# Performance work log

Hardware: AMD Instinct MI355X
Metric: run time of the kernel (lower is better)

Reference implementation:

```python
import jax, jax.numpy as jnp
import numpy as np

DIM = 1024
HEADS = 16
HEAD_DIM = DIM // HEADS          # 64
ROT_DIM = max(16, HEAD_DIM // 2) # 32 (already even)
B, S = 1, 2048


def _linear_params(key, scale=0.02):
    w = jax.random.normal(key, (DIM, DIM), dtype=jnp.float32) * scale
    b = jnp.zeros((DIM,), dtype=jnp.float32)
    return w, b


def setup_inputs() -> dict:
    key = jax.random.key(0)
    ks = jax.random.split(key, 16)
    real = jax.random.normal(ks[0], (B, S, DIM), dtype=jnp.float32)
    imag = jax.random.normal(ks[1], (B, S, DIM), dtype=jnp.float32)
    Wq_r, bq_r = _linear_params(ks[2])
    Wk_r, bk_r = _linear_params(ks[3])
    Wv_r, bv_r = _linear_params(ks[4])
    Wq_i, bq_i = _linear_params(ks[5])
    Wk_i, bk_i = _linear_params(ks[6])
    Wv_i, bv_i = _linear_params(ks[7])
    Wo_r, bo_r = _linear_params(ks[8])
    Wo_i, bo_i = _linear_params(ks[9])
    phase_shifts = jax.random.normal(ks[10], (HEADS, HEAD_DIM), dtype=jnp.float32) * 0.02
    # entanglement init: 0.8*I + 0.1 on super/sub diagonal + 0.1 corners
    ent = np.eye(HEADS, dtype=np.float32) * 0.8
    ent += np.diag(np.ones(HEADS - 1, dtype=np.float32) * 0.1, k=1)
    ent += np.diag(np.ones(HEADS - 1, dtype=np.float32) * 0.1, k=-1)
    ent[0, -1] = 0.1
    ent[-1, 0] = 0.1
    entanglement_matrix = jnp.asarray(ent)
    exponent = np.arange(0, ROT_DIM, 2, dtype=np.float64) / ROT_DIM
    rotary_freqs = jnp.asarray((10000.0 ** (-exponent)).astype(np.float32))
    return {
        'real': real, 'imag': imag,
        'Wq_r': Wq_r, 'bq_r': bq_r, 'Wk_r': Wk_r, 'bk_r': bk_r,
        'Wv_r': Wv_r, 'bv_r': bv_r, 'Wq_i': Wq_i, 'bq_i': bq_i,
        'Wk_i': Wk_i, 'bk_i': bk_i, 'Wv_i': Wv_i, 'bv_i': bv_i,
        'Wo_r': Wo_r, 'bo_r': bo_r, 'Wo_i': Wo_i, 'bo_i': bo_i,
        'phase_shifts': phase_shifts,
        'entanglement_matrix': entanglement_matrix,
        'rotary_freqs': rotary_freqs,
        'interference_strength': jnp.float32(0.0),
        'attention_temperature': jnp.float32(0.0),
        'circle_epsilon': jnp.float32(-2.0),
    }


def _proj(x, W, b):
    # nn.Linear: x @ W^T + b, then split heads -> [B,H,S,Dh]
    y = x @ W.T + b
    return y.reshape(B, S, HEADS, HEAD_DIM).transpose(0, 2, 1, 3)


def _rope(x, cos, sin):
    # x: [B,H,S,Dh]; interleaved pairs rotated over first ROT_DIM dims
    xr, xp = x[..., :ROT_DIM], x[..., ROT_DIM:]
    x1, x2 = xr[..., 0::2], xr[..., 1::2]          # [B,H,S,ROT_DIM//2]
    o1 = x1 * cos - x2 * sin
    o2 = x1 * sin + x2 * cos
    out = jnp.stack([o1, o2], axis=-1).reshape(x.shape[:-1] + (ROT_DIM,))
    return jnp.concatenate([out, xp], axis=-1)


def reference(real, imag, Wq_r, bq_r, Wk_r, bk_r, Wv_r, bv_r,
              Wq_i, bq_i, Wk_i, bk_i, Wv_i, bv_i,
              Wo_r, bo_r, Wo_i, bo_i,
              phase_shifts, entanglement_matrix, rotary_freqs,
              interference_strength, attention_temperature, circle_epsilon):
    q_r = _proj(real, Wq_r, bq_r)
    k_r = _proj(real, Wk_r, bk_r)
    v_r = _proj(real, Wv_r, bv_r)
    q_i = _proj(imag, Wq_i, bq_i)
    k_i = _proj(imag, Wk_i, bk_i)
    v_i = _proj(imag, Wv_i, bv_i)

    # rotary embeddings
    pos = jnp.arange(S, dtype=jnp.float32)
    angles = jnp.outer(pos, rotary_freqs)              # [S, ROT_DIM//2]
    cos = jnp.cos(angles)[None, None]                  # [1,1,S,ROT_DIM//2]
    sin = jnp.sin(angles)[None, None]
    q_r = _rope(q_r, cos, sin); k_r = _rope(k_r, cos, sin)
    q_i = _rope(q_i, cos, sin); k_i = _rope(k_i, cos, sin)

    # entanglement mixing across heads
    q_r = jnp.einsum('bhsd,hx->bxsd', q_r, entanglement_matrix)
    q_i = jnp.einsum('bhsd,hx->bxsd', q_i, entanglement_matrix)
    k_r = jnp.einsum('bhsd,hx->bxsd', k_r, entanglement_matrix)
    k_i = jnp.einsum('bhsd,hx->bxsd', k_i, entanglement_matrix)

    # per-head learned phase shift
    pc = jnp.cos(phase_shifts)[None, :, None, :]       # [1,H,1,Dh]
    ps = jnp.sin(phase_shifts)[None, :, None, :]
    q_r, q_i = q_r * pc - q_i * ps, q_r * ps + q_i * pc
    k_r, k_i = k_r * pc - k_i * ps, k_r * ps + k_i * pc

    # complex attention scores (Karatsuba, as in HAKMEMComplexOperations)
    scale = 1.0 / np.sqrt(HEAD_DIM)
    k1 = jnp.einsum('bhsd,bhtd->bhst', q_r, k_r)
    k2 = jnp.einsum('bhsd,bhtd->bhst', q_i, k_i)
    k3 = jnp.einsum('bhsd,bhtd->bhst', q_r + q_i, k_r + k_i)
    attn_r = (k1 - k2) * scale
    attn_i = (k3 - k1 - k2) * scale

    eps = jax.nn.sigmoid(circle_epsilon) * 0.03
    ar = attn_r + eps * attn_i
    ai = attn_i - eps * attn_r
    attn_mag = jnp.sqrt(ar * ar + ai * ai + 1e-6)

    causal = jnp.triu(jnp.ones((S, S), dtype=bool), k=1)[None, None]
    attn_mag = jnp.where(causal, -jnp.inf, attn_mag)

    temp = jnp.clip(jnp.exp(attention_temperature), 0.1, None)
    strength = jax.nn.sigmoid(interference_strength)
    attn = jax.nn.softmax(attn_mag * strength / temp, axis=-1)
    attn = jnp.nan_to_num(attn)

    # complex_matmul(attn, 0, v_r, v_i) -> (attn@v_r, attn@v_i)
    out_r = jnp.einsum('bhst,bhtd->bhsd', attn, v_r)
    out_i = jnp.einsum('bhst,bhtd->bhsd', attn, v_i)
    out_r = out_r.transpose(0, 2, 1, 3).reshape(B, S, DIM)
    out_i = out_i.transpose(0, 2, 1, 3).reshape(B, S, DIM)
    out_r = out_r @ Wo_r.T + bo_r
    out_i = out_i @ Wo_i.T + bo_i
    return out_r, out_i
```

## Files before the change

kernel.cpp:

```cpp
#include <hip/hip_runtime.h>
#include <cstddef>
#include <cstdint>
#include <math.h>

#define S_LEN 2048
#define DIM 1024
#define NH 16
#define HD 64

typedef __attribute__((ext_vector_type(8))) short bf16x8;
typedef __attribute__((ext_vector_type(8))) unsigned short u16x8;
typedef __attribute__((ext_vector_type(4))) float f32x4;

__device__ inline unsigned short f2bf(float x) {
  union { float f; unsigned u; } v; v.f = x;
  unsigned r = v.u + 0x7FFFu + ((v.u >> 16) & 1u);
  return (unsigned short)(r >> 16);
}
__device__ inline float bf2f(unsigned short x) {
  union { unsigned u; float f; } v; v.u = ((unsigned)x) << 16; return v.f;
}
__device__ inline unsigned pack_bf16_trunc(float hi, float lo) {
  union { float f; unsigned u; } a, b;
  a.f = hi; b.f = lo;
  return __builtin_amdgcn_perm(a.u, b.u, 0x07060302u);
}

#define GLOAD_LDS16(g, l)                                              \
  __builtin_amdgcn_global_load_lds(                                    \
      (const __attribute__((address_space(1))) void*)(g),              \
      (__attribute__((address_space(3))) void*)(l), 16, 0, 0)

struct ConvBatch {
  const float* src[6];
  unsigned short* dst[6];
  int n[6];
};

__global__ __launch_bounds__(256) void conv_kernel(
    ConvBatch cb, const float* __restrict__ E,
    const float* __restrict__ freqs, const float* __restrict__ phase,
    const float* __restrict__ bq_r, const float* __restrict__ bk_r,
    const float* __restrict__ bq_i, const float* __restrict__ bk_i,
    const float* __restrict__ Wq_r, const float* __restrict__ Wk_r,
    const float* __restrict__ Wq_i, const float* __restrict__ Wk_i,
    unsigned short* __restrict__ Wb,
    float* __restrict__ biasf, float2* __restrict__ ropeTab,
    float2* __restrict__ phaseTab2)
{
  const int t = threadIdx.x;
  const int y = blockIdx.y;

  if (y == 6) {
    __shared__ float Es[NH * NH];
    Es[t] = E[t];
    __syncthreads();
    const int idx = blockIdx.x * 256 + t;
    if (idx < 32768) {
      const int s = idx >> 4, j = idx & 15;
      float sn, cs;
      sincosf((float)s * freqs[j], &sn, &cs);
      ropeTab[idx] = make_float2(cs, sn);
    } else if (idx < 32768 + 1024) {
      const int k = idx - 32768;
      float sn, cs;
      sincosf(2.f * phase[k], &sn, &cs);
      phaseTab2[k] = make_float2(cs, sn);
    } else if (idx < 32768 + 1024 + 4096) {
      const int i = idx - 33792;
      const int tz = i >> 10, nn = i & 1023;
      const int x = nn >> 6, d = nn & 63;
      const float* b = (tz == 0) ? bq_r : (tz == 1) ? bk_r : (tz == 2) ? bq_i : bk_i;
      float acc = 0.f;
#pragma unroll
      for (int h = 0; h < NH; h++) acc += Es[h * NH + x] * b[h * 64 + d];
      biasf[i] = acc;
    }
    return;
  }

  if (y >= 7) {
    if (blockIdx.x >= 64) return;
    __shared__ float Es2[NH * NH];
    Es2[t] = E[t];
    __syncthreads();
    const int d  = blockIdx.x;
    const int wi = y - 7;
    const float* src = (wi == 0) ? Wq_r : (wi == 1) ? Wk_r : (wi == 2) ? Wq_i : Wk_i;
    const int slot   = (wi == 0) ? 0 : (wi == 1) ? 1 : (wi == 2) ? 3 : 4;
    unsigned short* dst = Wb + (size_t)slot * DIM * DIM;

    const int k0 = t * 4;
    float4 in[NH];
#pragma unroll
    for (int h = 0; h < NH; h++)
      in[h] = *(const float4*)(src + ((size_t)(h * 64 + d) << 10) + k0);

#pragma unroll
    for (int x = 0; x < NH; x++) {
      float ax = 0.f, ay = 0.f, az = 0.f, aw = 0.f;
#pragma unroll
      for (int h = 0; h < NH; h++) {
        const float e = Es2[h * NH + x];
        ax += e * in[h].x; ay += e * in[h].y;
        az += e * in[h].z; aw += e * in[h].w;
      }
      ushort4 o;
      o.x = f2bf(ax); o.y = f2bf(ay); o.z = f2bf(az); o.w = f2bf(aw);
      *(ushort4*)(dst + ((size_t)(x * 64 + d) << 10) + k0) = o;
    }
    return;
  }

  const int flat = (blockIdx.x * 256 + t) * 8;
  if (flat >= cb.n[y]) return;
  const float* s = cb.src[y];
  float4 a = *(const float4*)(s + flat);
  float4 b = *(const float4*)(s + flat + 4);
  u16x8 o;
  o[0] = f2bf(a.x); o[1] = f2bf(a.y); o[2] = f2bf(a.z); o[3] = f2bf(a.w);
  o[4] = f2bf(b.x); o[5] = f2bf(b.y); o[6] = f2bf(b.z); o[7] = f2bf(b.w);
  *(u16x8*)(cb.dst[y] + flat) = o;
}

struct BGemm {
  const unsigned short* A[6];
  const unsigned short* W[6];
  const float* bias[6];
  void* C[6];
  int mode[6];
  const float2* ropeTab;
};

__global__ __launch_bounds__(256) void gemm_mfma_kernel(BGemm gb)
{
  constexpr int K = DIM;
  const int z = blockIdx.z;
  const unsigned short* __restrict__ A = gb.A[z];
  const unsigned short* __restrict__ W = gb.W[z];
  const float* __restrict__ bias = gb.bias[z];
  const int mode = gb.mode[z];

  __shared__ __align__(16) unsigned short As[128 * 32];
  __shared__ __align__(16) unsigned short Ws[128 * 32];

  const int t    = threadIdx.x;
  const int lane = t & 63;
  const int w    = t >> 6;
  const int wm   = w >> 1, wn = w & 1;
  const int quad = lane >> 4, lcol = lane & 15;
  const int m0   = blockIdx.y * 128;
  const int n0   = blockIdx.x * 128;

  const int srow = t >> 2;
  const int sk8  = (t & 3) * 8;

  f32x4 acc[4][4];
#pragma unroll
  for (int i = 0; i < 4; i++)
#pragma unroll
    for (int j = 0; j < 4; j++)
#pragma unroll
      for (int r = 0; r < 4; r++) acc[i][j][r] = 0.f;

  for (int k0 = 0; k0 < K; k0 += 32) {
    __syncthreads();
#pragma unroll
    for (int p = 0; p < 2; p++) {
      const unsigned short* ga = A + (size_t)(m0 + p * 64 + srow) * K + k0 + sk8;
      GLOAD_LDS16(ga, As + (size_t)(p * 256 + w * 64) * 8);
      const unsigned short* gw = W + (size_t)(n0 + p * 64 + srow) * K + k0 + sk8;
      GLOAD_LDS16(gw, Ws + (size_t)(p * 256 + w * 64) * 8);
    }
    __syncthreads();

    bf16x8 af[4], bfr[4];
#pragma unroll
    for (int mi = 0; mi < 4; mi++)
      af[mi] = *(const bf16x8*)&As[(wm * 64 + mi * 16 + lcol) * 32 + quad * 8];
#pragma unroll
    for (int ni = 0; ni < 4; ni++)
      bfr[ni] = *(const bf16x8*)&Ws[(wn * 64 + ni * 16 + lcol) * 32 + quad * 8];
#pragma unroll
    for (int mi = 0; mi < 4; mi++)
#pragma unroll
      for (int ni = 0; ni < 4; ni++)
        acc[mi][ni] = __builtin_amdgcn_mfma_f32_16x16x32_bf16(af[mi], bfr[ni], acc[mi][ni], 0, 0, 0);
  }

#pragma unroll
  for (int mi = 0; mi < 4; mi++) {
#pragma unroll
    for (int ni = 0; ni < 4; ni++) {
#pragma unroll
      for (int r = 0; r < 4; r++) {
        const int grow = m0 + wm * 64 + mi * 16 + quad * 4 + r;
        const int gcol = n0 + wn * 64 + ni * 16 + lcol;
        float v = acc[mi][ni][r] + bias[gcol];
        if (mode == 3) {
          const float vp = __shfl_xor(v, 1);
          const int d = gcol & 63;
          if (d < 32) {
            const float2 cs = gb.ropeTab[grow * 16 + (d >> 1)];
            v = (d & 1) ? (v * cs.x + vp * cs.y)
                        : (v * cs.x - vp * cs.y);
          }
        }
        if (mode == 0) {
          ((float*)gb.C[z])[(size_t)grow * DIM + gcol] = v;
        } else if (mode == 2) {
          const int hh = gcol >> 6, d = gcol & 63;
          ((unsigned short*)gb.C[z])[((size_t)hh * HD + d) * S_LEN + grow] = f2bf(v);
        } else {
          const int hh = gcol >> 6, d = gcol & 63;
          ((unsigned short*)gb.C[z])[((size_t)hh * S_LEN + grow) * HD + d] = f2bf(v);
        }
      }
    }
  }
}

#define LDK 72

__global__ __launch_bounds__(256) void flash_mfma_kernel(
    const unsigned short* __restrict__ Qr, const unsigned short* __restrict__ Qi,
    const unsigned short* __restrict__ Kr, const unsigned short* __restrict__ Ki,
    const unsigned short* __restrict__ VtR, const unsigned short* __restrict__ VtI,
    unsigned short* __restrict__ OpR, unsigned short* __restrict__ OpI,
    float* __restrict__ Lp, const float2* __restrict__ phaseTab2,
    const float* __restrict__ p_is, const float* __restrict__ p_at,
    const float* __restrict__ p_ce)
{
  __shared__ __align__(16) unsigned short Krs[64 * LDK];
  __shared__ __align__(16) unsigned short Kis[64 * LDK];
  __shared__ __align__(16) unsigned short VTr[64 * LDK];
  __shared__ __align__(16) unsigned short VTi[64 * LDK];
  unsigned short* Ps = Krs;

  const int t    = threadIdx.x;
  const int lane = t & 63;
  const int w    = t >> 6;
  const int quad = lane >> 4;
  const int lcol = lane & 15;

  const int bx    = blockIdx.x;
  const int p     = bx >> 1;
  const int half  = bx & 1;
  const int itile = 31 - (p >> 4);
  const int h     = p & 15;
  const int i0    = itile * 64;
  const int n     = itile + 1;
  const int jmid  = (n + 1) >> 1;
  const int jbeg  = half ? jmid : 0;
  const int jend  = half ? n : jmid;

  const float strength = 1.f / (1.f + expf(-p_is[0]));
  const float temp     = fmaxf(expf(p_at[0]), 0.1f);
  const float cfac     = strength / temp;
  const float eps      = 0.03f / (1.f + expf(-p_ce[0]));
  const float c2       = 0.015625f * (1.f + eps * eps);
  const float cl       = cfac * 1.4426950408889634f;
  const float c2e      = c2 * cl * cl;
  const float epse     = 1e-6f * cl * cl;

  const int srow = t >> 3;
  const int sd0  = (t & 7) * 8;

  const int qg = i0 + w * 16 + lcol;

  bf16x8 qrf[2], qif[2];
  {
    const size_t base_q = ((size_t)h * S_LEN + qg) * HD;
#pragma unroll
    for (int ks = 0; ks < 2; ks++) {
      bf16x8 r8 = *(const bf16x8*)(Qr + base_q + ks * 32 + quad * 8);
      bf16x8 i8 = *(const bf16x8*)(Qi + base_q + ks * 32 + quad * 8);
      bf16x8 orr, oii;
#pragma unroll
      for (int j = 0; j < 8; j++) {
        const float2 ph = phaseTab2[h * HD + ks * 32 + quad * 8 + j];
        const float qr = bf2f((unsigned short)r8[j]);
        const float qi = bf2f((unsigned short)i8[j]);
        orr[j] = (short)f2bf(qr * ph.x - qi * ph.y);
        oii[j] = (short)f2bf(qr * ph.y + qi * ph.x);
      }
      qrf[ks] = orr;
      qif[ks] = oii;
    }
  }

  float lsum = 0.f;
  f32x4 aOr[4], aOi[4];
#pragma unroll
  for (int cc = 0; cc < 4; cc++)
#pragma unroll
    for (int r = 0; r < 4; r++) { aOr[cc][r] = 0.f; aOi[cc][r] = 0.f; }

  bf16x8 pk[2], pki[2], pv[2], pvi[2];

  const unsigned short* pKr = Kr  + ((size_t)h * S_LEN + jbeg * 64 + srow) * HD + sd0;
  const unsigned short* pKi = Ki  + ((size_t)h * S_LEN + jbeg * 64 + srow) * HD + sd0;
  const unsigned short* pVr = VtR + ((size_t)h * HD + srow) * S_LEN + jbeg * 64 + sd0;
  const unsigned short* pVi = VtI + ((size_t)h * HD + srow) * S_LEN + jbeg * 64 + sd0;

  if (jbeg < jend) {
#pragma unroll
    for (int it = 0; it < 2; it++) {
      pk [it] = *(const bf16x8*)(pKr + (size_t)it * 32 * HD);
      pki[it] = *(const bf16x8*)(pKi + (size_t)it * 32 * HD);
      pv [it] = *(const bf16x8*)(pVr + (size_t)it * 32 * S_LEN);
      pvi[it] = *(const bf16x8*)(pVi + (size_t)it * 32 * S_LEN);
    }
  }

  for (int jt = jbeg; jt < jend; jt++) {
    __syncthreads();
#pragma unroll
    for (int it = 0; it < 2; it++) {
      const int row = srow + it * 32;
      *(bf16x8*)&Krs[row * LDK + sd0] = pk [it];
      *(bf16x8*)&Kis[row * LDK + sd0] = pki[it];
      *(bf16x8*)&VTr[row * LDK + sd0] = pv [it];
      *(bf16x8*)&VTi[row * LDK + sd0] = pvi[it];
    }
    __syncthreads();

    if (jt + 1 < jend) {
      pKr += 64 * HD; pKi += 64 * HD; pVr += 64; pVi += 64;
#pragma unroll
      for (int it = 0; it < 2; it++) {
        pk [it] = *(const bf16x8*)(pKr + (size_t)it * 32 * HD);
        pki[it] = *(const bf16x8*)(pKi + (size_t)it * 32 * HD);
        pv [it] = *(const bf16x8*)(pVr + (size_t)it * 32 * S_LEN);
        pvi[it] = *(const bf16x8*)(pVi + (size_t)it * 32 * S_LEN);
      }
    }

    f32x4 k1[4], k2[4], kx[4];
#pragma unroll
    for (int cc = 0; cc < 4; cc++)
#pragma unroll
      for (int r = 0; r < 4; r++) { k1[cc][r] = 0.f; k2[cc][r] = 0.f; kx[cc][r] = 0.f; }
#pragma unroll
    for (int ks = 0; ks < 2; ks++) {
#pragma unroll
      for (int cc = 0; cc < 4; cc++) {
        const int off = (cc * 16 + lcol) * LDK + ks * 32 + quad * 8;
        bf16x8 krf = *(const bf16x8*)&Krs[off];
        bf16x8 kif = *(const bf16x8*)&Kis[off];
        k1[cc] = __builtin_amdgcn_mfma_f32_16x16x32_bf16(krf, qrf[ks], k1[cc], 0, 0, 0);
        k2[cc] = __builtin_amdgcn_mfma_f32_16x16x32_bf16(kif, qif[ks], k2[cc], 0, 0, 0);
        kx[cc] = __builtin_amdgcn_mfma_f32_16x16x32_bf16(kif, qrf[ks], kx[cc], 0, 0, 0);
        kx[cc] = __builtin_amdgcn_mfma_f32_16x16x32_bf16(krf, qif[ks], kx[cc], 0, 0, 0);
      }
    }

    __syncthreads();

    const int prow = (w * 16 + lcol) * LDK;
    if (jt != itile) {
#pragma unroll
      for (int cc = 0; cc < 4; cc++) {
        float pv4[4];
#pragma unroll
        for (int r = 0; r < 4; r++) {
          const float a = k1[cc][r] - k2[cc][r];
          const float b = kx[cc][r];
          const float u = fmaf(b, b, a * a);
          const float pp = __builtin_amdgcn_exp2f(sqrtf(fmaf(u, c2e, epse)));
          pv4[r] = pp;
          lsum += pp;
        }
        uint2 packed;
        packed.x = pack_bf16_trunc(pv4[1], pv4[0]);
        packed.y = pack_bf16_trunc(pv4[3], pv4[2]);
        *(uint2*)&Ps[prow + cc * 16 + quad * 4] = packed;
      }
    } else {
      const int j0 = jt * 64;
#pragma unroll
      for (int cc = 0; cc < 4; cc++) {
        float pv4[4];
#pragma unroll
        for (int r = 0; r < 4; r++) {
          const float a = k1[cc][r] - k2[cc][r];
          const float b = kx[cc][r];
          const float u = fmaf(b, b, a * a);
          float pp = __builtin_amdgcn_exp2f(sqrtf(fmaf(u, c2e, epse)));
          const int gj = j0 + cc * 16 + quad * 4 + r;
          if (gj > qg) pp = 0.f;
          pv4[r] = pp;
          lsum += pp;
        }
        uint2 packed;
        packed.x = pack_bf16_trunc(pv4[1], pv4[0]);
        packed.y = pack_bf16_trunc(pv4[3], pv4[2]);
        *(uint2*)&Ps[prow + cc * 16 + quad * 4] = packed;
      }
    }

#pragma unroll
    for (int ks = 0; ks < 2; ks++) {
      bf16x8 pf = *(const bf16x8*)&Ps[(w * 16 + lcol) * LDK + ks * 32 + quad * 8];
#pragma unroll
      for (int cc = 0; cc < 4; cc++) {
        const int off = (cc * 16 + lcol) * LDK + ks * 32 + quad * 8;
        bf16x8 vrf = *(const bf16x8*)&VTr[off];
        bf16x8 vif = *(const bf16x8*)&VTi[off];
        aOr[cc] = __builtin_amdgcn_mfma_f32_16x16x32_bf16(vrf, pf, aOr[cc], 0, 0, 0);
        aOi[cc] = __builtin_amdgcn_mfma_f32_16x16x32_bf16(vif, pf, aOi[cc], 0, 0, 0);
      }
    }
  }

  lsum += __shfl_xor(lsum, 16);
  lsum += __shfl_xor(lsum, 32);
  if (lane < 16)
    Lp[((size_t)half * NH + h) * S_LEN + qg] = lsum;

  const size_t SLsz = (size_t)S_LEN * DIM;
  const size_t rowbase = half * SLsz + (size_t)qg * DIM + h * HD;
#pragma unroll
  for (int cc = 0; cc < 4; cc++) {
    const int d0 = cc * 16 + quad * 4;
    uint2 pr, pi;
    pr.x = pack_bf16_trunc(aOr[cc][1], aOr[cc][0]);
    pr.y = pack_bf16_trunc(aOr[cc][3], aOr[cc][2]);
    pi.x = pack_bf16_trunc(aOi[cc][1], aOi[cc][0]);
    pi.y = pack_bf16_trunc(aOi[cc][3], aOi[cc][2]);
    *(uint2*)(OpR + rowbase + d0) = pr;
    *(uint2*)(OpI + rowbase + d0) = pi;
  }
}

__global__ __launch_bounds__(256) void combine_kernel(
    const unsigned short* __restrict__ OpR, const unsigned short* __restrict__ OpI,
    const float* __restrict__ Lp,
    unsigned short* __restrict__ Or, unsigned short* __restrict__ Oi)
{
  const size_t SLsz = (size_t)S_LEN * DIM;
  const int idx = blockIdx.x * 256 + threadIdx.x;
  const size_t e0 = (size_t)idx * 8;
  const int s = (int)(e0 >> 10);
  const int col = (int)(e0 & 1023);
  const int h = col >> 6;

  const float L = Lp[(size_t)h * S_LEN + s] + Lp[((size_t)NH + h) * S_LEN + s];
  const float inv = 1.f / L;

  bf16x8 r0 = *(const bf16x8*)(OpR + e0);
  bf16x8 r1 = *(const bf16x8*)(OpR + SLsz + e0);
  bf16x8 i0 = *(const bf16x8*)(OpI + e0);
  bf16x8 i1 = *(const bf16x8*)(OpI + SLsz + e0);

  u16x8 orv, oiv;
#pragma unroll
  for (int j = 0; j < 8; j++) {
    orv[j] = f2bf((bf2f((unsigned short)r0[j]) + bf2f((unsigned short)r1[j])) * inv);
    oiv[j] = f2bf((bf2f((unsigned short)i0[j]) + bf2f((unsigned short)i1[j])) * inv);
  }
  *(u16x8*)(Or + e0) = orv;
  *(u16x8*)(Oi + e0) = oiv;
}

extern "C" void kernel_launch(void* const* d_in, const int* in_sizes, int n_in,
                              void* d_out, int out_size, void* d_ws, size_t ws_size,
                              hipStream_t stream)
{
  const float* real = (const float*)d_in[0];
  const float* imag = (const float*)d_in[1];
  const float* Wq_r = (const float*)d_in[2];
  const float* bq_r = (const float*)d_in[3];
  const float* Wk_r = (const float*)d_in[4];
  const float* bk_r = (const float*)d_in[5];
  const float* Wv_r = (const float*)d_in[6];
  const float* bv_r = (const float*)d_in[7];
  const float* Wq_i = (const float*)d_in[8];
  const float* bq_i = (const float*)d_in[9];
  const float* Wk_i = (const float*)d_in[10];
  const float* bk_i = (const float*)d_in[11];
  const float* Wv_i = (const float*)d_in[12];
  const float* bv_i = (const float*)d_in[13];
  const float* Wo_r = (const float*)d_in[14];
  const float* bo_r = (const float*)d_in[15];
  const float* Wo_i = (const float*)d_in[16];
  const float* bo_i = (const float*)d_in[17];
  const float* phase = (const float*)d_in[18];
  const float* ent   = (const float*)d_in[19];
  const float* freqs = (const float*)d_in[20];
  const float* p_is  = (const float*)d_in[21];
  const float* p_at  = (const float*)d_in[22];
  const float* p_ce  = (const float*)d_in[23];

  unsigned short* ws = (unsigned short*)d_ws;
  const size_t SL = (size_t)S_LEN * DIM;
  const size_t WL = (size_t)DIM * DIM;

  unsigned short* realb = ws;
  unsigned short* imagb = realb + SL;
  unsigned short* Wb    = imagb + SL;
  unsigned short* q_r   = Wb + 8 * WL;
  unsigned short* k_r   = q_r + SL;
  unsigned short* v_r   = k_r + SL;
  unsigned short* q_i   = v_r + SL;
  unsigned short* k_i   = q_i + SL;
  unsigned short* v_i   = k_i + SL;
  unsigned short* OpR   = v_i + SL;
  unsigned short* OpI   = OpR + 2 * SL;

  float* fbase    = (float*)(OpI + 2 * SL);
  float* biasf    = fbase;
  float* ropeTab  = biasf + 4096;
  float* phaseTb2 = ropeTab + 65536;
  float* Lp       = phaseTb2 + 2048;

  unsigned short* O_r = q_r;
  unsigned short* O_i = q_i;

  float* out_r = (float*)d_out;
  float* out_i = out_r + SL;

  ConvBatch cb;
  cb.src[0] = real;  cb.dst[0] = realb;        cb.n[0] = (int)SL;
  cb.src[1] = imag;  cb.dst[1] = imagb;        cb.n[1] = (int)SL;
  cb.src[2] = Wv_r;  cb.dst[2] = Wb + 2 * WL;  cb.n[2] = (int)WL;
  cb.src[3] = Wv_i;  cb.dst[3] = Wb + 5 * WL;  cb.n[3] = (int)WL;
  cb.src[4] = Wo_r;  cb.dst[4] = Wb + 6 * WL;  cb.n[4] = (int)WL;
  cb.src[5] = Wo_i;  cb.dst[5] = Wb + 7 * WL;  cb.n[5] = (int)WL;
  conv_kernel<<<dim3(1024, 11), dim3(256), 0, stream>>>(
      cb, ent, freqs, phase, bq_r, bk_r, bq_i, bk_i,
      Wq_r, Wk_r, Wq_i, Wk_i, Wb,
      biasf, (float2*)ropeTab, (float2*)phaseTb2);

  BGemm g1;
  g1.A[0] = realb; g1.A[1] = realb; g1.A[2] = realb;
  g1.A[3] = imagb; g1.A[4] = imagb; g1.A[5] = imagb;
  for (int i = 0; i < 6; i++) g1.W[i] = Wb + (size_t)i * WL;
  g1.bias[0] = biasf;        g1.bias[1] = biasf + 1024; g1.bias[2] = bv_r;
  g1.bias[3] = biasf + 2048; g1.bias[4] = biasf + 3072; g1.bias[5] = bv_i;
  g1.C[0] = q_r; g1.C[1] = k_r; g1.C[2] = v_r;
  g1.C[3] = q_i; g1.C[4] = k_i; g1.C[5] = v_i;
  g1.mode[0] = 3; g1.mode[1] = 3; g1.mode[2] = 2;
  g1.mode[3] = 3; g1.mode[4] = 3; g1.mode[5] = 2;
  g1.ropeTab = (const float2*)ropeTab;
  gemm_mfma_kernel<<<dim3(8, 16, 6), dim3(256), 0, stream>>>(g1);

  flash_mfma_kernel<<<dim3(1024), dim3(256), 0, stream>>>(
      q_r, q_i, k_r, k_i, v_r, v_i, OpR, OpI, Lp,
      (const float2*)phaseTb2, p_is, p_at, p_ce);

  combine_kernel<<<dim3(1024), dim3(256), 0, stream>>>(OpR, OpI, Lp, O_r, O_i);

  BGemm g2 = {};
  g2.A[0] = O_r; g2.A[1] = O_i;
  g2.W[0] = Wb + 6 * WL; g2.W[1] = Wb + 7 * WL;
  g2.bias[0] = bo_r; g2.bias[1] = bo_i;
  g2.C[0] = out_r; g2.C[1] = out_i;
  g2.mode[0] = 0; g2.mode[1] = 0;
  g2.ropeTab = (const float2*)ropeTab;
  gemm_mfma_kernel<<<dim3(8, 16, 2), dim3(256), 0, stream>>>(g2);
}
```

Measured before the change: 273.6 us.

## Split causal attention KV range into four chunks with paired job scheduling

The attention kernel now splits each query tile's key range into four chunks instead of two, and each block processes two jobs, blockIdx and its mirror 2047-blockIdx, to even out causal work across blocks. The combine kernel sums four partial outputs and four partial row sums, and the workspace partial buffers double in size. This targets load imbalance from the causal triangle, at the cost of more partial-result traffic in the combine step and extra Q reloads per job.

```diff
diff --git a/kernel.cpp b/kernel.cpp
--- a/kernel.cpp
+++ b/kernel.cpp
@@ -243,17 +243,6 @@
   const int quad = lane >> 4;
   const int lcol = lane & 15;
 
-  const int bx    = blockIdx.x;
-  const int p     = bx >> 1;
-  const int half  = bx & 1;
-  const int itile = 31 - (p >> 4);
-  const int h     = p & 15;
-  const int i0    = itile * 64;
-  const int n     = itile + 1;
-  const int jmid  = (n + 1) >> 1;
-  const int jbeg  = half ? jmid : 0;
-  const int jend  = half ? n : jmid;
-
   const float strength = 1.f / (1.f + expf(-p_is[0]));
   const float temp     = fmaxf(expf(p_at[0]), 0.1f);
   const float cfac     = strength / temp;
@@ -265,68 +254,57 @@
 
   const int srow = t >> 3;
   const int sd0  = (t & 7) * 8;
-
-  const int qg = i0 + w * 16 + lcol;
-
-  bf16x8 qrf[2], qif[2];
-  {
-    const size_t base_q = ((size_t)h * S_LEN + qg) * HD;
-#pragma unroll
-    for (int ks = 0; ks < 2; ks++) {
-      bf16x8 r8 = *(const bf16x8*)(Qr + base_q + ks * 32 + quad * 8);
-      bf16x8 i8 = *(const bf16x8*)(Qi + base_q + ks * 32 + quad * 8);
-      bf16x8 orr, oii;
-#pragma unroll
-      for (int j = 0; j < 8; j++) {
-        const float2 ph = phaseTab2[h * HD + ks * 32 + quad * 8 + j];
-        const float qr = bf2f((unsigned short)r8[j]);
-        const float qi = bf2f((unsigned short)i8[j]);
-        orr[j] = (short)f2bf(qr * ph.x - qi * ph.y);
-        oii[j] = (short)f2bf(qr * ph.y + qi * ph.x);
-      }
-      qrf[ks] = orr;
-      qif[ks] = oii;
-    }
-  }
-
-  float lsum = 0.f;
-  f32x4 aOr[4], aOi[4];
-#pragma unroll
-  for (int cc = 0; cc < 4; cc++)
-#pragma unroll
-    for (int r = 0; r < 4; r++) { aOr[cc][r] = 0.f; aOi[cc][r] = 0.f; }
-
-  bf16x8 pk[2], pki[2], pv[2], pvi[2];
-
-  const unsigned short* pKr = Kr  + ((size_t)h * S_LEN + jbeg * 64 + srow) * HD + sd0;
-  const unsigned short* pKi = Ki  + ((size_t)h * S_LEN + jbeg * 64 + srow) * HD + sd0;
-  const unsigned short* pVr = VtR + ((size_t)h * HD + srow) * S_LEN + jbeg * 64 + sd0;
-  const unsigned short* pVi = VtI + ((size_t)h * HD + srow) * S_LEN + jbeg * 64 + sd0;
-
-  if (jbeg < jend) {
-#pragma unroll
-    for (int it = 0; it < 2; it++) {
-      pk [it] = *(const bf16x8*)(pKr + (size_t)it * 32 * HD);
-      pki[it] = *(const bf16x8*)(pKi + (size_t)it * 32 * HD);
-      pv [it] = *(const bf16x8*)(pVr + (size_t)it * 32 * S_LEN);
-      pvi[it] = *(const bf16x8*)(pVi + (size_t)it * 32 * S_LEN);
-    }
-  }
-
-  for (int jt = jbeg; jt < jend; jt++) {
-    __syncthreads();
-#pragma unroll
-    for (int it = 0; it < 2; it++) {
-      const int row = srow + it * 32;
-      *(bf16x8*)&Krs[row * LDK + sd0] = pk [it];
-      *(bf16x8*)&Kis[row * LDK + sd0] = pki[it];
-      *(bf16x8*)&VTr[row * LDK + sd0] = pv [it];
-      *(bf16x8*)&VTi[row * LDK + sd0] = pvi[it];
-    }
-    __syncthreads();
-
-    if (jt + 1 < jend) {
-      pKr += 64 * HD; pKi += 64 * HD; pVr += 64; pVi += 64;
+  const size_t SLsz = (size_t)S_LEN * DIM;
+
+  for (int jj = 0; jj < 2; jj++) {
+    const int job   = jj ? (2047 - (int)blockIdx.x) : (int)blockIdx.x;
+    const int p     = job >> 2;
+    const int q     = job & 3;
+    const int itile = 31 - (p >> 4);
+    const int h     = p & 15;
+    const int i0    = itile * 64;
+    const int n     = itile + 1;
+    const int jbeg  = (n * q) >> 2;
+    const int jend  = (n * (q + 1)) >> 2;
+
+    const int qg = i0 + w * 16 + lcol;
+
+    bf16x8 qrf[2], qif[2];
+    {
+      const size_t base_q = ((size_t)h * S_LEN + qg) * HD;
+#pragma unroll
+      for (int ks = 0; ks < 2; ks++) {
+        bf16x8 r8 = *(const bf16x8*)(Qr + base_q + ks * 32 + quad * 8);
+        bf16x8 i8 = *(const bf16x8*)(Qi + base_q + ks * 32 + quad * 8);
+        bf16x8 orr, oii;
+#pragma unroll
+        for (int j = 0; j < 8; j++) {
+          const float2 ph = phaseTab2[h * HD + ks * 32 + quad * 8 + j];
+          const float qr = bf2f((unsigned short)r8[j]);
+          const float qi = bf2f((unsigned short)i8[j]);
+          orr[j] = (short)f2bf(qr * ph.x - qi * ph.y);
+          oii[j] = (short)f2bf(qr * ph.y + qi * ph.x);
+        }
+        qrf[ks] = orr;
+        qif[ks] = oii;
+      }
+    }
+
+    float lsum = 0.f;
+    f32x4 aOr[4], aOi[4];
+#pragma unroll
+    for (int cc = 0; cc < 4; cc++)
+#pragma unroll
+      for (int r = 0; r < 4; r++) { aOr[cc][r] = 0.f; aOi[cc][r] = 0.f; }
+
+    bf16x8 pk[2], pki[2], pv[2], pvi[2];
+
+    const unsigned short* pKr = Kr  + ((size_t)h * S_LEN + jbeg * 64 + srow) * HD + sd0;
+    const unsigned short* pKi = Ki  + ((size_t)h * S_LEN + jbeg * 64 + srow) * HD + sd0;
+    const unsigned short* pVr = VtR + ((size_t)h * HD + srow) * S_LEN + jbeg * 64 + sd0;
+    const unsigned short* pVi = VtI + ((size_t)h * HD + srow) * S_LEN + jbeg * 64 + sd0;
+
+    if (jbeg < jend) {
 #pragma unroll
       for (int it = 0; it < 2; it++) {
         pk [it] = *(const bf16x8*)(pKr + (size_t)it * 32 * HD);
@@ -336,100 +314,123 @@
       }
     }
 
-    f32x4 k1[4], k2[4], kx[4];
-#pragma unroll
-    for (int cc = 0; cc < 4; cc++)
-#pragma unroll
-      for (int r = 0; r < 4; r++) { k1[cc][r] = 0.f; k2[cc][r] = 0.f; kx[cc][r] = 0.f; }
-#pragma unroll
-    for (int ks = 0; ks < 2; ks++) {
-#pragma unroll
-      for (int cc = 0; cc < 4; cc++) {
-        const int off = (cc * 16 + lcol) * LDK + ks * 32 + quad * 8;
-        bf16x8 krf = *(const bf16x8*)&Krs[off];
-        bf16x8 kif = *(const bf16x8*)&Kis[off];
-        k1[cc] = __builtin_amdgcn_mfma_f32_16x16x32_bf16(krf, qrf[ks], k1[cc], 0, 0, 0);
-        k2[cc] = __builtin_amdgcn_mfma_f32_16x16x32_bf16(kif, qif[ks], k2[cc], 0, 0, 0);
-        kx[cc] = __builtin_amdgcn_mfma_f32_16x16x32_bf16(kif, qrf[ks], kx[cc], 0, 0, 0);
-        kx[cc] = __builtin_amdgcn_mfma_f32_16x16x32_bf16(krf, qif[ks], kx[cc], 0, 0, 0);
-      }
-    }
-
-    __syncthreads();
-
-    const int prow = (w * 16 + lcol) * LDK;
-    if (jt != itile) {
-#pragma unroll
-      for (int cc = 0; cc < 4; cc++) {
-        float pv4[4];
-#pragma unroll
-        for (int r = 0; r < 4; r++) {
-          const float a = k1[cc][r] - k2[cc][r];
-          const float b = kx[cc][r];
-          const float u = fmaf(b, b, a * a);
-          const float pp = __builtin_amdgcn_exp2f(sqrtf(fmaf(u, c2e, epse)));
-          pv4[r] = pp;
-          lsum += pp;
-        }
-        uint2 packed;
-        packed.x = pack_bf16_trunc(pv4[1], pv4[0]);
-        packed.y = pack_bf16_trunc(pv4[3], pv4[2]);
-        *(uint2*)&Ps[prow + cc * 16 + quad * 4] = packed;
-      }
-    } else {
-      const int j0 = jt * 64;
-#pragma unroll
-      for (int cc = 0; cc < 4; cc++) {
-        float pv4[4];
-#pragma unroll
-        for (int r = 0; r < 4; r++) {
-          const float a = k1[cc][r] - k2[cc][r];
-          const float b = kx[cc][r];
-          const float u = fmaf(b, b, a * a);
-          float pp = __builtin_amdgcn_exp2f(sqrtf(fmaf(u, c2e, epse)));
-          const int gj = j0 + cc * 16 + quad * 4 + r;
-          if (gj > qg) pp = 0.f;
-          pv4[r] = pp;
-          lsum += pp;
-        }
-        uint2 packed;
-        packed.x = pack_bf16_trunc(pv4[1], pv4[0]);
-        packed.y = pack_bf16_trunc(pv4[3], pv4[2]);
-        *(uint2*)&Ps[prow + cc * 16 + quad * 4] = packed;
-      }
-    }
-
-#pragma unroll
-    for (int ks = 0; ks < 2; ks++) {
-      bf16x8 pf = *(const bf16x8*)&Ps[(w * 16 + lcol) * LDK + ks * 32 + quad * 8];
-#pragma unroll
-      for (int cc = 0; cc < 4; cc++) {
-        const int off = (cc * 16 + lcol) * LDK + ks * 32 + quad * 8;
-        bf16x8 vrf = *(const bf16x8*)&VTr[off];
-        bf16x8 vif = *(const bf16x8*)&VTi[off];
-        aOr[cc] = __builtin_amdgcn_mfma_f32_16x16x32_bf16(vrf, pf, aOr[cc], 0, 0, 0);
-        aOi[cc] = __builtin_amdgcn_mfma_f32_16x16x32_bf16(vif, pf, aOi[cc], 0, 0, 0);
-      }
-    }
-  }
-
-  lsum += __shfl_xor(lsum, 16);
-  lsum += __shfl_xor(lsum, 32);
-  if (lane < 16)
-    Lp[((size_t)half * NH + h) * S_LEN + qg] = lsum;
-
-  const size_t SLsz = (size_t)S_LEN * DIM;
-  const size_t rowbase = half * SLsz + (size_t)qg * DIM + h * HD;
-#pragma unroll
-  for (int cc = 0; cc < 4; cc++) {
-    const int d0 = cc * 16 + quad * 4;
-    uint2 pr, pi;
-    pr.x = pack_bf16_trunc(aOr[cc][1], aOr[cc][0]);
-    pr.y = pack_bf16_trunc(aOr[cc][3], aOr[cc][2]);
-    pi.x = pack_bf16_trunc(aOi[cc][1], aOi[cc][0]);
-    pi.y = pack_bf16_trunc(aOi[cc][3], aOi[cc][2]);
-    *(uint2*)(OpR + rowbase + d0) = pr;
-    *(uint2*)(OpI + rowbase + d0) = pi;
+    for (int jt = jbeg; jt < jend; jt++) {
+      __syncthreads();
+#pragma unroll
+      for (int it = 0; it < 2; it++) {
+        const int row = srow + it * 32;
+        *(bf16x8*)&Krs[row * LDK + sd0] = pk [it];
+        *(bf16x8*)&Kis[row * LDK + sd0] = pki[it];
+        *(bf16x8*)&VTr[row * LDK + sd0] = pv [it];
+        *(bf16x8*)&VTi[row * LDK + sd0] = pvi[it];
+      }
+      __syncthreads();
+
+      if (jt + 1 < jend) {
+        pKr += 64 * HD; pKi += 64 * HD; pVr += 64; pVi += 64;
+#pragma unroll
+        for (int it = 0; it < 2; it++) {
+          pk [it] = *(const bf16x8*)(pKr + (size_t)it * 32 * HD);
+          pki[it] = *(const bf16x8*)(pKi + (size_t)it * 32 * HD);
+          pv [it] = *(const bf16x8*)(pVr + (size_t)it * 32 * S_LEN);
+          pvi[it] = *(const bf16x8*)(pVi + (size_t)it * 32 * S_LEN);
+        }
+      }
+
+      f32x4 k1[4], k2[4], kx[4];
+#pragma unroll
+      for (int cc = 0; cc < 4; cc++)
+#pragma unroll
+        for (int r = 0; r < 4; r++) { k1[cc][r] = 0.f; k2[cc][r] = 0.f; kx[cc][r] = 0.f; }
+#pragma unroll
+      for (int ks = 0; ks < 2; ks++) {
+#pragma unroll
+        for (int cc = 0; cc < 4; cc++) {
+          const int off = (cc * 16 + lcol) * LDK + ks * 32 + quad * 8;
+          bf16x8 krf = *(const bf16x8*)&Krs[off];
+          bf16x8 kif = *(const bf16x8*)&Kis[off];
+          k1[cc] = __builtin_amdgcn_mfma_f32_16x16x32_bf16(krf, qrf[ks], k1[cc], 0, 0, 0);
+          k2[cc] = __builtin_amdgcn_mfma_f32_16x16x32_bf16(kif, qif[ks], k2[cc], 0, 0, 0);
+          kx[cc] = __builtin_amdgcn_mfma_f32_16x16x32_bf16(kif, qrf[ks], kx[cc], 0, 0, 0);
+          kx[cc] = __builtin_amdgcn_mfma_f32_16x16x32_bf16(krf, qif[ks], kx[cc], 0, 0, 0);
+        }
+      }
+
+      __syncthreads();
+
+      const int prow = (w * 16 + lcol) * LDK;
+      if (jt != itile) {
+#pragma unroll
+        for (int cc = 0; cc < 4; cc++) {
+          float pv4[4];
+#pragma unroll
+          for (int r = 0; r < 4; r++) {
+            const float a = k1[cc][r] - k2[cc][r];
+            const float b = kx[cc][r];
+            const float u = fmaf(b, b, a * a);
+            const float pp = __builtin_amdgcn_exp2f(sqrtf(fmaf(u, c2e, epse)));
+            pv4[r] = pp;
+            lsum += pp;
+          }
+          uint2 packed;
+          packed.x = pack_bf16_trunc(pv4[1], pv4[0]);
+          packed.y = pack_bf16_trunc(pv4[3], pv4[2]);
+          *(uint2*)&Ps[prow + cc * 16 + quad * 4] = packed;
+        }
+      } else {
+        const int j0 = jt * 64;
+#pragma unroll
+        for (int cc = 0; cc < 4; cc++) {
+          float pv4[4];
+#pragma unroll
+          for (int r = 0; r < 4; r++) {
+            const float a = k1[cc][r] - k2[cc][r];
+            const float b = kx[cc][r];
+            const float u = fmaf(b, b, a * a);
+            float pp = __builtin_amdgcn_exp2f(sqrtf(fmaf(u, c2e, epse)));
+            const int gj = j0 + cc * 16 + quad * 4 + r;
+            if (gj > qg) pp = 0.f;
+            pv4[r] = pp;
+            lsum += pp;
+          }
+          uint2 packed;
+          packed.x = pack_bf16_trunc(pv4[1], pv4[0]);
+          packed.y = pack_bf16_trunc(pv4[3], pv4[2]);
+          *(uint2*)&Ps[prow + cc * 16 + quad * 4] = packed;
+        }
+      }
+
+#pragma unroll
+      for (int ks = 0; ks < 2; ks++) {
+        bf16x8 pf = *(const bf16x8*)&Ps[(w * 16 + lcol) * LDK + ks * 32 + quad * 8];
+#pragma unroll
+        for (int cc = 0; cc < 4; cc++) {
+          const int off = (cc * 16 + lcol) * LDK + ks * 32 + quad * 8;
+          bf16x8 vrf = *(const bf16x8*)&VTr[off];
+          bf16x8 vif = *(const bf16x8*)&VTi[off];
+          aOr[cc] = __builtin_amdgcn_mfma_f32_16x16x32_bf16(vrf, pf, aOr[cc], 0, 0, 0);
+          aOi[cc] = __builtin_amdgcn_mfma_f32_16x16x32_bf16(vif, pf, aOi[cc], 0, 0, 0);
+        }
+      }
+    }
+
+    lsum += __shfl_xor(lsum, 16);
+    lsum += __shfl_xor(lsum, 32);
+    if (lane < 16)
+      Lp[((size_t)q * NH + h) * S_LEN + qg] = lsum;
+
+    const size_t rowbase = (size_t)q * SLsz + (size_t)qg * DIM + h * HD;
+#pragma unroll
+    for (int cc = 0; cc < 4; cc++) {
+      const int d0 = cc * 16 + quad * 4;
+      uint2 pr, pi;
+      pr.x = pack_bf16_trunc(aOr[cc][1], aOr[cc][0]);
+      pr.y = pack_bf16_trunc(aOr[cc][3], aOr[cc][2]);
+      pi.x = pack_bf16_trunc(aOi[cc][1], aOi[cc][0]);
+      pi.y = pack_bf16_trunc(aOi[cc][3], aOi[cc][2]);
+      *(uint2*)(OpR + rowbase + d0) = pr;
+      *(uint2*)(OpI + rowbase + d0) = pi;
+    }
   }
 }
 
@@ -445,19 +446,29 @@
   const int col = (int)(e0 & 1023);
   const int h = col >> 6;
 
-  const float L = Lp[(size_t)h * S_LEN + s] + Lp[((size_t)NH + h) * S_LEN + s];
+  float L = 0.f;
+#pragma unroll
+  for (int q = 0; q < 4; q++)
+    L += Lp[((size_t)q * NH + h) * S_LEN + s];
   const float inv = 1.f / L;
 
-  bf16x8 r0 = *(const bf16x8*)(OpR + e0);
-  bf16x8 r1 = *(const bf16x8*)(OpR + SLsz + e0);
-  bf16x8 i0 = *(const bf16x8*)(OpI + e0);
-  bf16x8 i1 = *(const bf16x8*)(OpI + SLsz + e0);
+  float accR[8] = {}, accI[8] = {};
+#pragma unroll
+  for (int q = 0; q < 4; q++) {
+    bf16x8 rq = *(const bf16x8*)(OpR + (size_t)q * SLsz + e0);
+    bf16x8 iq = *(const bf16x8*)(OpI + (size_t)q * SLsz + e0);
+#pragma unroll
+    for (int j = 0; j < 8; j++) {
+      accR[j] += bf2f((unsigned short)rq[j]);
+      accI[j] += bf2f((unsigned short)iq[j]);
+    }
+  }
 
   u16x8 orv, oiv;
 #pragma unroll
   for (int j = 0; j < 8; j++) {
-    orv[j] = f2bf((bf2f((unsigned short)r0[j]) + bf2f((unsigned short)r1[j])) * inv);
-    oiv[j] = f2bf((bf2f((unsigned short)i0[j]) + bf2f((unsigned short)i1[j])) * inv);
+    orv[j] = f2bf(accR[j] * inv);
+    oiv[j] = f2bf(accI[j] * inv);
   }
   *(u16x8*)(Or + e0) = orv;
   *(u16x8*)(Oi + e0) = oiv;
@@ -506,9 +517,9 @@
   unsigned short* k_i   = q_i + SL;
   unsigned short* v_i   = k_i + SL;
   unsigned short* OpR   = v_i + SL;
-  unsigned short* OpI   = OpR + 2 * SL;
-
-  float* fbase    = (float*)(OpI + 2 * SL);
+  unsigned short* OpI   = OpR + 4 * SL;
+
+  float* fbase    = (float*)(OpI + 4 * SL);
   float* biasf    = fbase;
   float* ropeTab  = biasf + 4096;
   float* phaseTb2 = ropeTab + 65536;
```

After: 287.7 us. 1.05x slower.
